# Kernel tuning notes

Measured on AMD Instinct MI355X. Metric: run time of the kernel, lower is better.

## Reference

```python
import jax, jax.numpy as jnp
import numpy as np

N, F, A = 50000, 128, 128

def setup_inputs() -> dict:
    key = jax.random.key(0)
    ks = jax.random.split(key, 20)
    r = lambda i, shape: jax.random.normal(ks[i], shape, dtype=jnp.float32)
    w = lambda i, shape: jax.random.normal(ks[i], shape, dtype=jnp.float32) * 0.05
    return {
        "feat": r(0, (N, F)),
        "mu": r(1, (N, F, 3)),
        "T0": r(2, (N,)),
        "T1": r(3, (N, 3)),
        "T2": r(4, (N, 3, 3)),
        "T3": r(5, (N, 3, 3, 3)),
        # denseq: Dense(F,F,swish) -> Dense(F,F). Weights stored [in,out].
        "Wq1": w(6, (F, F)), "bq1": jnp.zeros((F,), jnp.float32),
        "Wq2": w(7, (F, F)), "bq2": jnp.zeros((F,), jnp.float32),
        "WT1": w(8, (F, F)),  # dense_T1, no bias
        "WT2": w(9, (F, F)),  # dense_T2, no bias
        "WT3": w(10, (F, F)), # dense_T3, no bias
        # dense_s: Dense(F,F,swish) -> Dense(F,A)
        "Ws1": w(11, (F, F)), "bs1": jnp.zeros((F,), jnp.float32),
        "Ws2": w(12, (F, A)), "bs2": jnp.zeros((A,), jnp.float32),
        "Wv": w(13, (F, A)),  # dense_v, no bias
    }

def reference(feat, mu, T0, T1, T2, T3,
              Wq1, bq1, Wq2, bq2, WT1, WT2, WT3,
              Ws1, bs1, Ws2, bs2, Wv):
    silu = jax.nn.silu  # swish
    # M0 = denseq(feat): [N, F]
    M0 = silu(feat @ Wq1 + bq1) @ Wq2 + bq2
    # M1/M2/M3: linear over feature dim of mu [N, F, 3]
    M1 = jnp.einsum('nfc,fg->ngc', mu, WT1)
    M2 = jnp.einsum('nfc,fg->ngc', mu, WT2)
    M3 = jnp.einsum('nfc,fg->ngc', mu, WT3)
    # scalar channel
    ms = jnp.sum(M1 * T1[:, None, :], axis=-1) + T0[:, None] * M0          # T1, T0 terms
    ms = ms + jnp.einsum('nfi,nfj,nij->nf', M2, M2, T2)                    # quadrupole . T2
    ms = ms + jnp.einsum('nfi,nfj,nfk,nijk->nf', M3, M3, M3, T3)           # octupole . T3
    # vector channel [N, F, 3]
    mv = T1[:, None, :] * M0[..., None]
    mv = mv + jnp.einsum('nij,nfj->nfi', T2, M1)
    mv = mv + jnp.einsum('nijk,nfj,nfk->nfi', T3, M2, M2)
    # output projections
    mv_out = jnp.einsum('nfc,fa->nac', mv, Wv)                             # [N, A, 3]
    ms_out = silu(ms @ Ws1 + bs1) @ Ws2 + bs2                              # [N, A]
    return ms_out, mv_out
```

## Files before the change

kernel.cpp:

```cpp
#include <hip/hip_runtime.h>
#include <cstdint>

#define N_NODES 50000
#define TILE 32
#define NBLK ((N_NODES + TILE - 1) / TILE)

typedef __bf16 bf16x8 __attribute__((ext_vector_type(8)));
typedef unsigned short ushort8_t __attribute__((ext_vector_type(8)));
typedef float f32x4 __attribute__((ext_vector_type(4)));

__device__ __forceinline__ unsigned short f2bf(float x) {
  union { float f; uint32_t u; } v; v.f = x;
  uint32_t r = v.u + 0x7FFFu + ((v.u >> 16) & 1u);
  return (unsigned short)(r >> 16);
}

__device__ __forceinline__ float fast_silu(float x) {
  return x / (1.0f + __expf(-x));
}

__global__ __launch_bounds__(256) void prep_weights(
    const float* __restrict__ Wq1, const float* __restrict__ Wq2,
    const float* __restrict__ WT1, const float* __restrict__ WT2,
    const float* __restrict__ WT3, const float* __restrict__ Ws1,
    const float* __restrict__ Ws2, const float* __restrict__ Wv,
    unsigned short* __restrict__ ws) {
  int tid = blockIdx.x * 256 + threadIdx.x;
  int w = tid >> 11;
  int rest = tid & 2047;
  int c = rest >> 8;
  int kt = (rest >> 6) & 3;
  int lane = rest & 63;
  int g = (lane & 15) + 16 * c;
  int k0 = kt * 32 + (lane >> 4) * 8;
  const float* srcs[8] = {Wq1, Wq2, WT1, WT2, WT3, Ws1, Ws2, Wv};
  const float* src = srcs[w];
  union { unsigned short u[8]; uint4 v; } o;
#pragma unroll
  for (int j = 0; j < 8; ++j) o.u[j] = f2bf(src[(k0 + j) * 128 + g]);
  *(uint4*)(ws + (size_t)w * 16384 + (size_t)rest * 8) = o.v;
}

__device__ __forceinline__ void gemm16(const unsigned short* sA,
                                       const unsigned short* sWp,
                                       int lane, int cb, f32x4 acc[2][2]) {
  const int m = lane & 15, q = lane >> 4;
  const f32x4 vzero = {0.f, 0.f, 0.f, 0.f};
#pragma unroll
  for (int rt = 0; rt < 2; ++rt)
#pragma unroll
    for (int cc = 0; cc < 2; ++cc) acc[rt][cc] = vzero;
#pragma unroll
  for (int kt = 0; kt < 4; ++kt) {
    const int k0 = q * 8 + kt * 32;
    bf16x8 a0 = __builtin_bit_cast(bf16x8, *(const ushort8_t*)(sA + m * 136 + k0));
    bf16x8 a1 = __builtin_bit_cast(bf16x8, *(const ushort8_t*)(sA + (m + 16) * 136 + k0));
#pragma unroll
    for (int cc = 0; cc < 2; ++cc) {
      bf16x8 b = __builtin_bit_cast(
          bf16x8, *(const ushort8_t*)(sWp + (((cb + cc) * 4 + kt) * 64 + lane) * 8));
      acc[0][cc] = __builtin_amdgcn_mfma_f32_16x16x32_bf16(a0, b, acc[0][cc], 0, 0, 0);
      acc[1][cc] = __builtin_amdgcn_mfma_f32_16x16x32_bf16(a1, b, acc[1][cc], 0, 0, 0);
    }
  }
}

__global__ __launch_bounds__(256, 2) void multipole_main(
    const float* __restrict__ feat, const float* __restrict__ mu,
    const float* __restrict__ T0g, const float* __restrict__ T1g,
    const float* __restrict__ T2g, const float* __restrict__ T3g,
    const float* __restrict__ bq1, const float* __restrict__ bq2,
    const float* __restrict__ bs1, const float* __restrict__ bs2,
    const unsigned short* __restrict__ ws, float* __restrict__ out) {
  __shared__ unsigned short sW[16384];
  __shared__ unsigned short sXmain[TILE * 136];
  __shared__ unsigned short sXmu[3][TILE * 136];
  __shared__ float sT[TILE][49];

  const int t = threadIdx.x;
  const int lane = t & 63, wv = t >> 6;
  const int m = lane & 15, q = lane >> 4;
  const int cb = wv * 2;
  const int nodeBase = blockIdx.x * TILE;

  auto stage_w = [&](int slot) {
    const uint4* src = (const uint4*)(ws + (size_t)slot * 16384);
    uint4* dst = (uint4*)sW;
#pragma unroll
    for (int i = 0; i < 8; ++i) dst[t + i * 256] = src[t + i * 256];
  };

  if (t < TILE) {
    int n = nodeBase + t;
    bool val = n < N_NODES;
    float t0 = val ? T0g[n] : 0.f;
    float t1[3], t2[9], t3[27];
#pragma unroll
    for (int i = 0; i < 3; ++i) t1[i] = val ? T1g[n * 3 + i] : 0.f;
#pragma unroll
    for (int i = 0; i < 9; ++i) t2[i] = val ? T2g[n * 9 + i] : 0.f;
#pragma unroll
    for (int i = 0; i < 27; ++i) t3[i] = val ? T3g[n * 27 + i] : 0.f;
    float* Tr = sT[t];
    Tr[0] = t0;
    Tr[1] = t1[0]; Tr[2] = t1[1]; Tr[3] = t1[2];
#pragma unroll
    for (int i = 0; i < 9; ++i) Tr[4 + i] = t2[i];
    Tr[13] = t2[0]; Tr[14] = t2[1] + t2[3]; Tr[15] = t2[2] + t2[6];
    Tr[16] = t2[4]; Tr[17] = t2[5] + t2[7]; Tr[18] = t2[8];
    Tr[19] = t3[0];
    Tr[20] = t3[1] + t3[3] + t3[9];
    Tr[21] = t3[2] + t3[6] + t3[18];
    Tr[22] = t3[4] + t3[10] + t3[12];
    Tr[23] = t3[5] + t3[7] + t3[11] + t3[15] + t3[19] + t3[21];
    Tr[24] = t3[8] + t3[20] + t3[24];
    Tr[25] = t3[13];
    Tr[26] = t3[14] + t3[16] + t3[22];
    Tr[27] = t3[17] + t3[23] + t3[25];
    Tr[28] = t3[26];
#pragma unroll
    for (int i = 0; i < 3; ++i) {
      const float* b = t3 + 9 * i;
      float* d = Tr + 29 + 6 * i;
      d[0] = b[0]; d[1] = b[1] + b[3]; d[2] = b[2] + b[6];
      d[3] = b[4]; d[4] = b[5] + b[7]; d[5] = b[8];
    }
  }

  {
    int node = t >> 3, f0 = (t & 7) * 16;
    int gn = nodeBase + node;
    union { unsigned short u[16]; uint4 v[2]; } buf;
    if (gn < N_NODES) {
      const float* p = feat + (size_t)gn * 128 + f0;
#pragma unroll
      for (int i = 0; i < 16; ++i) buf.u[i] = f2bf(p[i]);
    } else {
#pragma unroll
      for (int i = 0; i < 16; ++i) buf.u[i] = 0;
    }
    uint4* dst = (uint4*)&sXmain[node * 136 + f0];
    dst[0] = buf.v[0]; dst[1] = buf.v[1];
  }
  stage_w(0);
  __syncthreads();

  f32x4 A1[2][2], A2[2][2], A3[2][2];
  float msv[2][2][4];
  float mvv[3][2][2][4];

  gemm16(sXmain, sW, lane, cb, A1);
  float b0 = bq1[cb * 16 + m], b1 = bq1[cb * 16 + 16 + m];
  __syncthreads();
#pragma unroll
  for (int rt = 0; rt < 2; ++rt)
#pragma unroll
    for (int ri = 0; ri < 4; ++ri) {
      int lrow = rt * 16 + q * 4 + ri;
#pragma unroll
      for (int cc = 0; cc < 2; ++cc) {
        float h = fast_silu(A1[rt][cc][ri] + (cc ? b1 : b0));
        sXmain[lrow * 136 + (cb + cc) * 16 + m] = f2bf(h);
      }
    }
  stage_w(1);
  __syncthreads();

  gemm16(sXmain, sW, lane, cb, A1);
  {
    float bb0 = bq2[cb * 16 + m], bb1 = bq2[cb * 16 + 16 + m];
#pragma unroll
    for (int rt = 0; rt < 2; ++rt)
#pragma unroll
      for (int ri = 0; ri < 4; ++ri) {
        const float* Tr = sT[rt * 16 + q * 4 + ri];
        float t0 = Tr[0], ta = Tr[1], tb = Tr[2], tc = Tr[3];
#pragma unroll
        for (int cc = 0; cc < 2; ++cc) {
          float m0 = A1[rt][cc][ri] + (cc ? bb1 : bb0);
          msv[rt][cc][ri] = t0 * m0;
          mvv[0][rt][cc][ri] = ta * m0;
          mvv[1][rt][cc][ri] = tb * m0;
          mvv[2][rt][cc][ri] = tc * m0;
        }
      }
  }
  __syncthreads();

  {
    int node = t >> 3, f0 = (t & 7) * 16;
    int gn = nodeBase + node;
    union { unsigned short u[16]; uint4 v[2]; } b3[3];
    if (gn < N_NODES) {
      const float* p = mu + ((size_t)gn * 128 + f0) * 3;
#pragma unroll
      for (int i = 0; i < 16; ++i) {
        b3[0].u[i] = f2bf(p[i * 3 + 0]);
        b3[1].u[i] = f2bf(p[i * 3 + 1]);
        b3[2].u[i] = f2bf(p[i * 3 + 2]);
      }
    } else {
#pragma unroll
      for (int ch = 0; ch < 3; ++ch)
#pragma unroll
        for (int i = 0; i < 16; ++i) b3[ch].u[i] = 0;
    }
#pragma unroll
    for (int ch = 0; ch < 3; ++ch) {
      uint4* dst = (uint4*)&sXmu[ch][node * 136 + f0];
      dst[0] = b3[ch].v[0]; dst[1] = b3[ch].v[1];
    }
  }
  stage_w(2);
  __syncthreads();

#pragma unroll
  for (int ch = 0; ch < 3; ++ch) {
    gemm16(sXmu[ch], sW, lane, cb, A1);
#pragma unroll
    for (int rt = 0; rt < 2; ++rt)
#pragma unroll
      for (int ri = 0; ri < 4; ++ri) {
        const float* Tr = sT[rt * 16 + q * 4 + ri];
        float t1c = Tr[1 + ch];
        float u0 = Tr[4 + 0 + ch], u1 = Tr[4 + 3 + ch], u2 = Tr[4 + 6 + ch];
#pragma unroll
        for (int cc = 0; cc < 2; ++cc) {
          float v = A1[rt][cc][ri];
          msv[rt][cc][ri] += t1c * v;
          mvv[0][rt][cc][ri] += u0 * v;
          mvv[1][rt][cc][ri] += u1 * v;
          mvv[2][rt][cc][ri] += u2 * v;
        }
      }
  }
  __syncthreads();
  stage_w(4);
  __syncthreads();

  gemm16(sXmu[0], sW, lane, cb, A1);
  gemm16(sXmu[1], sW, lane, cb, A2);
  gemm16(sXmu[2], sW, lane, cb, A3);
#pragma unroll
  for (int rt = 0; rt < 2; ++rt)
#pragma unroll
    for (int ri = 0; ri < 4; ++ri) {
      const float* Cp = sT[rt * 16 + q * 4 + ri] + 19;
      float c0 = Cp[0], c1 = Cp[1], c2 = Cp[2], c3 = Cp[3], c4 = Cp[4];
      float c5 = Cp[5], c6 = Cp[6], c7 = Cp[7], c8 = Cp[8], c9 = Cp[9];
#pragma unroll
      for (int cc = 0; cc < 2; ++cc) {
        float u0 = A1[rt][cc][ri], u1 = A2[rt][cc][ri], u2 = A3[rt][cc][ri];
        float Q0 = u0 * u0, Q1 = u0 * u1, Q2 = u0 * u2;
        float Q3 = u1 * u1, Q4 = u1 * u2, Q5 = u2 * u2;
        msv[rt][cc][ri] += c0 * (Q0 * u0) + c1 * (Q0 * u1) + c2 * (Q0 * u2) +
                           c3 * (Q1 * u1) + c4 * (Q1 * u2) + c5 * (Q2 * u2) +
                           c6 * (Q3 * u1) + c7 * (Q3 * u2) + c8 * (Q4 * u2) +
                           c9 * (Q5 * u2);
      }
    }
  __syncthreads();
  stage_w(3);
  __syncthreads();

  gemm16(sXmu[0], sW, lane, cb, A1);
  gemm16(sXmu[1], sW, lane, cb, A2);
  gemm16(sXmu[2], sW, lane, cb, A3);
#pragma unroll
  for (int rt = 0; rt < 2; ++rt)
#pragma unroll
    for (int ri = 0; ri < 4; ++ri) {
      const float* Tr = sT[rt * 16 + q * 4 + ri];
      const float* q2 = Tr + 13;
      const float* d3 = Tr + 29;
      float q20 = q2[0], q21 = q2[1], q22 = q2[2], q23 = q2[3], q24 = q2[4], q25 = q2[5];
#pragma unroll
      for (int cc = 0; cc < 2; ++cc) {
        float v0 = A1[rt][cc][ri], v1 = A2[rt][cc][ri], v2 = A3[rt][cc][ri];
        float P0 = v0 * v0, P1 = v0 * v1, P2 = v0 * v2;
        float P3 = v1 * v1, P4 = v1 * v2, P5 = v2 * v2;
        msv[rt][cc][ri] += q20 * P0 + q21 * P1 + q22 * P2 + q23 * P3 + q24 * P4 + q25 * P5;
        mvv[0][rt][cc][ri] += d3[0] * P0 + d3[1] * P1 + d3[2] * P2 + d3[3] * P3 + d3[4] * P4 + d3[5] * P5;
        mvv[1][rt][cc][ri] += d3[6] * P0 + d3[7] * P1 + d3[8] * P2 + d3[9] * P3 + d3[10] * P4 + d3[11] * P5;
        mvv[2][rt][cc][ri] += d3[12] * P0 + d3[13] * P1 + d3[14] * P2 + d3[15] * P3 + d3[16] * P4 + d3[17] * P5;
      }
    }
  __syncthreads();

#pragma unroll
  for (int rt = 0; rt < 2; ++rt)
#pragma unroll
    for (int ri = 0; ri < 4; ++ri) {
      int lrow = rt * 16 + q * 4 + ri;
#pragma unroll
      for (int cc = 0; cc < 2; ++cc) {
        int col = (cb + cc) * 16 + m;
        sXmain[lrow * 136 + col] = f2bf(msv[rt][cc][ri]);
        sXmu[0][lrow * 136 + col] = f2bf(mvv[0][rt][cc][ri]);
        sXmu[1][lrow * 136 + col] = f2bf(mvv[1][rt][cc][ri]);
        sXmu[2][lrow * 136 + col] = f2bf(mvv[2][rt][cc][ri]);
      }
    }
  stage_w(5);
  __syncthreads();

  gemm16(sXmain, sW, lane, cb, A1);
  {
    float s0 = bs1[cb * 16 + m], s1 = bs1[cb * 16 + 16 + m];
    __syncthreads();
#pragma unroll
    for (int rt = 0; rt < 2; ++rt)
#pragma unroll
      for (int ri = 0; ri < 4; ++ri) {
        int lrow = rt * 16 + q * 4 + ri;
#pragma unroll
        for (int cc = 0; cc < 2; ++cc) {
          float g = fast_silu(A1[rt][cc][ri] + (cc ? s1 : s0));
          sXmain[lrow * 136 + (cb + cc) * 16 + m] = f2bf(g);
        }
      }
  }
  stage_w(6);
  __syncthreads();

  gemm16(sXmain, sW, lane, cb, A1);
  {
    float s0 = bs2[cb * 16 + m], s1 = bs2[cb * 16 + 16 + m];
#pragma unroll
    for (int rt = 0; rt < 2; ++rt)
#pragma unroll
      for (int ri = 0; ri < 4; ++ri) {
        int grow = nodeBase + rt * 16 + q * 4 + ri;
        if (grow < N_NODES) {
#pragma unroll
          for (int cc = 0; cc < 2; ++cc) {
            int col = (cb + cc) * 16 + m;
            out[(size_t)grow * 128 + col] = A1[rt][cc][ri] + (cc ? s1 : s0);
          }
        }
      }
  }
  __syncthreads();
  stage_w(7);
  __syncthreads();

  float* out2 = out + (size_t)N_NODES * 128;
#pragma unroll
  for (int ch = 0; ch < 3; ++ch) {
    gemm16(sXmu[ch], sW, lane, cb, A1);
#pragma unroll
    for (int rt = 0; rt < 2; ++rt)
#pragma unroll
      for (int ri = 0; ri < 4; ++ri) {
        int grow = nodeBase + rt * 16 + q * 4 + ri;
        if (grow < N_NODES) {
#pragma unroll
          for (int cc = 0; cc < 2; ++cc) {
            int col = (cb + cc) * 16 + m;
            out2[((size_t)grow * 128 + col) * 3 + ch] = A1[rt][cc][ri];
          }
        }
      }
  }
}

extern "C" void kernel_launch(void* const* d_in, const int* in_sizes, int n_in,
                              void* d_out, int out_size, void* d_ws, size_t ws_size,
                              hipStream_t stream) {
  const float* feat = (const float*)d_in[0];
  const float* mu   = (const float*)d_in[1];
  const float* T0   = (const float*)d_in[2];
  const float* T1   = (const float*)d_in[3];
  const float* T2   = (const float*)d_in[4];
  const float* T3   = (const float*)d_in[5];
  const float* Wq1  = (const float*)d_in[6];
  const float* bq1  = (const float*)d_in[7];
  const float* Wq2  = (const float*)d_in[8];
  const float* bq2  = (const float*)d_in[9];
  const float* WT1  = (const float*)d_in[10];
  const float* WT2  = (const float*)d_in[11];
  const float* WT3  = (const float*)d_in[12];
  const float* Ws1  = (const float*)d_in[13];
  const float* bs1  = (const float*)d_in[14];
  const float* Ws2  = (const float*)d_in[15];
  const float* bs2  = (const float*)d_in[16];
  const float* Wv   = (const float*)d_in[17];
  unsigned short* ws = (unsigned short*)d_ws;
  float* out = (float*)d_out;

  prep_weights<<<64, 256, 0, stream>>>(Wq1, Wq2, WT1, WT2, WT3, Ws1, Ws2, Wv, ws);
  multipole_main<<<NBLK, 256, 0, stream>>>(feat, mu, T0, T1, T2, T3,
                                           bq1, bq2, bs1, bs2, ws, out);
}
```

Measured before the change: 275.8 us.

## Read MFMA weight fragments from global memory instead of staging through LDS

Removes the 32KB shared weight buffer and its per-stage copies and barriers. MFMA B fragments now load directly from the prepacked global workspace, where they should hit L2 or cache. This frees LDS and raises the occupancy target to 4 blocks per CU. Input loads for feat and mu are vectorized as float4 and hoisted to the kernel start, and the final Wv projection is fused across the three channels so all three components of each output are written together. The risk is extra global/L2 traffic and load latency on every GEMM.

```diff
diff --git a/kernel.cpp b/kernel.cpp
--- a/kernel.cpp
+++ b/kernel.cpp
@@ -41,9 +41,15 @@
   *(uint4*)(ws + (size_t)w * 16384 + (size_t)rest * 8) = o.v;
 }
 
-__device__ __forceinline__ void gemm16(const unsigned short* sA,
-                                       const unsigned short* sWp,
-                                       int lane, int cb, f32x4 acc[2][2]) {
+__device__ __forceinline__ bf16x8 ldB(const unsigned short* __restrict__ wg,
+                                      int c, int kt, int lane) {
+  return __builtin_bit_cast(
+      bf16x8, *(const ushort8_t*)(wg + (((c * 4 + kt) * 64 + lane)) * 8));
+}
+
+__device__ __forceinline__ void gemm16g(const unsigned short* __restrict__ sA,
+                                        const unsigned short* __restrict__ wg,
+                                        int lane, int cb, f32x4 acc[2][2]) {
   const int m = lane & 15, q = lane >> 4;
   const f32x4 vzero = {0.f, 0.f, 0.f, 0.f};
 #pragma unroll
@@ -57,25 +63,60 @@
     bf16x8 a1 = __builtin_bit_cast(bf16x8, *(const ushort8_t*)(sA + (m + 16) * 136 + k0));
 #pragma unroll
     for (int cc = 0; cc < 2; ++cc) {
-      bf16x8 b = __builtin_bit_cast(
-          bf16x8, *(const ushort8_t*)(sWp + (((cb + cc) * 4 + kt) * 64 + lane) * 8));
+      bf16x8 b = ldB(wg, cb + cc, kt, lane);
       acc[0][cc] = __builtin_amdgcn_mfma_f32_16x16x32_bf16(a0, b, acc[0][cc], 0, 0, 0);
       acc[1][cc] = __builtin_amdgcn_mfma_f32_16x16x32_bf16(a1, b, acc[1][cc], 0, 0, 0);
     }
   }
 }
 
-__global__ __launch_bounds__(256, 2) void multipole_main(
+__device__ __forceinline__ void gemm3g(const unsigned short* __restrict__ s0,
+                                       const unsigned short* __restrict__ s1,
+                                       const unsigned short* __restrict__ s2,
+                                       const unsigned short* __restrict__ wg,
+                                       int lane, int cb,
+                                       f32x4 A1[2][2], f32x4 A2[2][2],
+                                       f32x4 A3[2][2]) {
+  const int m = lane & 15, q = lane >> 4;
+  const f32x4 vzero = {0.f, 0.f, 0.f, 0.f};
+#pragma unroll
+  for (int rt = 0; rt < 2; ++rt)
+#pragma unroll
+    for (int cc = 0; cc < 2; ++cc) {
+      A1[rt][cc] = vzero; A2[rt][cc] = vzero; A3[rt][cc] = vzero;
+    }
+#pragma unroll
+  for (int kt = 0; kt < 4; ++kt) {
+    const int k0 = q * 8 + kt * 32;
+    bf16x8 a00 = __builtin_bit_cast(bf16x8, *(const ushort8_t*)(s0 + m * 136 + k0));
+    bf16x8 a01 = __builtin_bit_cast(bf16x8, *(const ushort8_t*)(s0 + (m + 16) * 136 + k0));
+    bf16x8 a10 = __builtin_bit_cast(bf16x8, *(const ushort8_t*)(s1 + m * 136 + k0));
+    bf16x8 a11 = __builtin_bit_cast(bf16x8, *(const ushort8_t*)(s1 + (m + 16) * 136 + k0));
+    bf16x8 a20 = __builtin_bit_cast(bf16x8, *(const ushort8_t*)(s2 + m * 136 + k0));
+    bf16x8 a21 = __builtin_bit_cast(bf16x8, *(const ushort8_t*)(s2 + (m + 16) * 136 + k0));
+#pragma unroll
+    for (int cc = 0; cc < 2; ++cc) {
+      bf16x8 b = ldB(wg, cb + cc, kt, lane);
+      A1[0][cc] = __builtin_amdgcn_mfma_f32_16x16x32_bf16(a00, b, A1[0][cc], 0, 0, 0);
+      A1[1][cc] = __builtin_amdgcn_mfma_f32_16x16x32_bf16(a01, b, A1[1][cc], 0, 0, 0);
+      A2[0][cc] = __builtin_amdgcn_mfma_f32_16x16x32_bf16(a10, b, A2[0][cc], 0, 0, 0);
+      A2[1][cc] = __builtin_amdgcn_mfma_f32_16x16x32_bf16(a11, b, A2[1][cc], 0, 0, 0);
+      A3[0][cc] = __builtin_amdgcn_mfma_f32_16x16x32_bf16(a20, b, A3[0][cc], 0, 0, 0);
+      A3[1][cc] = __builtin_amdgcn_mfma_f32_16x16x32_bf16(a21, b, A3[1][cc], 0, 0, 0);
+    }
+  }
+}
+
+__global__ __launch_bounds__(256, 4) void multipole_main(
     const float* __restrict__ feat, const float* __restrict__ mu,
     const float* __restrict__ T0g, const float* __restrict__ T1g,
     const float* __restrict__ T2g, const float* __restrict__ T3g,
     const float* __restrict__ bq1, const float* __restrict__ bq2,
     const float* __restrict__ bs1, const float* __restrict__ bs2,
     const unsigned short* __restrict__ ws, float* __restrict__ out) {
-  __shared__ unsigned short sW[16384];
   __shared__ unsigned short sXmain[TILE * 136];
   __shared__ unsigned short sXmu[3][TILE * 136];
-  __shared__ float sT[TILE][49];
+  __shared__ float sT[TILE][47];
 
   const int t = threadIdx.x;
   const int lane = t & 63, wv = t >> 6;
@@ -83,12 +124,52 @@
   const int cb = wv * 2;
   const int nodeBase = blockIdx.x * TILE;
 
-  auto stage_w = [&](int slot) {
-    const uint4* src = (const uint4*)(ws + (size_t)slot * 16384);
-    uint4* dst = (uint4*)sW;
-#pragma unroll
-    for (int i = 0; i < 8; ++i) dst[t + i * 256] = src[t + i * 256];
-  };
+  {
+    int node = t >> 3, f0 = (t & 7) * 16;
+    int gn = nodeBase + node;
+    union { unsigned short u[16]; uint4 v[2]; } buf;
+    if (gn < N_NODES) {
+      const float4* p = (const float4*)(feat + (size_t)gn * 128 + f0);
+      float xs[16];
+#pragma unroll
+      for (int i = 0; i < 4; ++i) *(float4*)(xs + 4 * i) = p[i];
+#pragma unroll
+      for (int i = 0; i < 16; ++i) buf.u[i] = f2bf(xs[i]);
+    } else {
+#pragma unroll
+      for (int i = 0; i < 16; ++i) buf.u[i] = 0;
+    }
+    uint4* dst = (uint4*)&sXmain[node * 136 + f0];
+    dst[0] = buf.v[0]; dst[1] = buf.v[1];
+  }
+
+  {
+    int node = t >> 3, f0 = (t & 7) * 16;
+    int gn = nodeBase + node;
+    union { unsigned short u[16]; uint4 v[2]; } b3[3];
+    if (gn < N_NODES) {
+      const float4* p = (const float4*)(mu + ((size_t)gn * 128 + f0) * 3);
+      float xs[48];
+#pragma unroll
+      for (int i = 0; i < 12; ++i) *(float4*)(xs + 4 * i) = p[i];
+#pragma unroll
+      for (int i = 0; i < 16; ++i) {
+        b3[0].u[i] = f2bf(xs[i * 3 + 0]);
+        b3[1].u[i] = f2bf(xs[i * 3 + 1]);
+        b3[2].u[i] = f2bf(xs[i * 3 + 2]);
+      }
+    } else {
+#pragma unroll
+      for (int ch = 0; ch < 3; ++ch)
+#pragma unroll
+        for (int i = 0; i < 16; ++i) b3[ch].u[i] = 0;
+    }
+#pragma unroll
+    for (int ch = 0; ch < 3; ++ch) {
+      uint4* dst = (uint4*)&sXmu[ch][node * 136 + f0];
+      dst[0] = b3[ch].v[0]; dst[1] = b3[ch].v[1];
+    }
+  }
 
   if (t < TILE) {
     int n = nodeBase + t;
@@ -126,30 +207,13 @@
       d[3] = b[4]; d[4] = b[5] + b[7]; d[5] = b[8];
     }
   }
-
-  {
-    int node = t >> 3, f0 = (t & 7) * 16;
-    int gn = nodeBase + node;
-    union { unsigned short u[16]; uint4 v[2]; } buf;
-    if (gn < N_NODES) {
-      const float* p = feat + (size_t)gn * 128 + f0;
-#pragma unroll
-      for (int i = 0; i < 16; ++i) buf.u[i] = f2bf(p[i]);
-    } else {
-#pragma unroll
-      for (int i = 0; i < 16; ++i) buf.u[i] = 0;
-    }
-    uint4* dst = (uint4*)&sXmain[node * 136 + f0];
-    dst[0] = buf.v[0]; dst[1] = buf.v[1];
-  }
-  stage_w(0);
   __syncthreads();
 
   f32x4 A1[2][2], A2[2][2], A3[2][2];
   float msv[2][2][4];
   float mvv[3][2][2][4];
 
-  gemm16(sXmain, sW, lane, cb, A1);
+  gemm16g(sXmain, ws, lane, cb, A1);
   float b0 = bq1[cb * 16 + m], b1 = bq1[cb * 16 + 16 + m];
   __syncthreads();
 #pragma unroll
@@ -163,10 +227,9 @@
         sXmain[lrow * 136 + (cb + cc) * 16 + m] = f2bf(h);
       }
     }
-  stage_w(1);
-  __syncthreads();
-
-  gemm16(sXmain, sW, lane, cb, A1);
+  __syncthreads();
+
+  gemm16g(sXmain, ws + 1 * 16384, lane, cb, A1);
   {
     float bb0 = bq2[cb * 16 + m], bb1 = bq2[cb * 16 + 16 + m];
 #pragma unroll
@@ -185,38 +248,10 @@
         }
       }
   }
-  __syncthreads();
-
-  {
-    int node = t >> 3, f0 = (t & 7) * 16;
-    int gn = nodeBase + node;
-    union { unsigned short u[16]; uint4 v[2]; } b3[3];
-    if (gn < N_NODES) {
-      const float* p = mu + ((size_t)gn * 128 + f0) * 3;
-#pragma unroll
-      for (int i = 0; i < 16; ++i) {
-        b3[0].u[i] = f2bf(p[i * 3 + 0]);
-        b3[1].u[i] = f2bf(p[i * 3 + 1]);
-        b3[2].u[i] = f2bf(p[i * 3 + 2]);
-      }
-    } else {
-#pragma unroll
-      for (int ch = 0; ch < 3; ++ch)
-#pragma unroll
-        for (int i = 0; i < 16; ++i) b3[ch].u[i] = 0;
-    }
-#pragma unroll
-    for (int ch = 0; ch < 3; ++ch) {
-      uint4* dst = (uint4*)&sXmu[ch][node * 136 + f0];
-      dst[0] = b3[ch].v[0]; dst[1] = b3[ch].v[1];
-    }
-  }
-  stage_w(2);
-  __syncthreads();
 
 #pragma unroll
   for (int ch = 0; ch < 3; ++ch) {
-    gemm16(sXmu[ch], sW, lane, cb, A1);
+    gemm16g(sXmu[ch], ws + 2 * 16384, lane, cb, A1);
 #pragma unroll
     for (int rt = 0; rt < 2; ++rt)
 #pragma unroll
@@ -234,13 +269,10 @@
         }
       }
   }
-  __syncthreads();
-  stage_w(4);
-  __syncthreads();
-
-  gemm16(sXmu[0], sW, lane, cb, A1);
-  gemm16(sXmu[1], sW, lane, cb, A2);
-  gemm16(sXmu[2], sW, lane, cb, A3);
+
+  gemm16g(sXmu[0], ws + 4 * 16384, lane, cb, A1);
+  gemm16g(sXmu[1], ws + 4 * 16384, lane, cb, A2);
+  gemm16g(sXmu[2], ws + 4 * 16384, lane, cb, A3);
 #pragma unroll
   for (int rt = 0; rt < 2; ++rt)
 #pragma unroll
@@ -259,13 +291,10 @@
                            c9 * (Q5 * u2);
       }
     }
-  __syncthreads();
-  stage_w(3);
-  __syncthreads();
-
-  gemm16(sXmu[0], sW, lane, cb, A1);
-  gemm16(sXmu[1], sW, lane, cb, A2);
-  gemm16(sXmu[2], sW, lane, cb, A3);
+
+  gemm16g(sXmu[0], ws + 3 * 16384, lane, cb, A1);
+  gemm16g(sXmu[1], ws + 3 * 16384, lane, cb, A2);
+  gemm16g(sXmu[2], ws + 3 * 16384, lane, cb, A3);
 #pragma unroll
   for (int rt = 0; rt < 2; ++rt)
 #pragma unroll
@@ -301,10 +330,9 @@
         sXmu[2][lrow * 136 + col] = f2bf(mvv[2][rt][cc][ri]);
       }
     }
-  stage_w(5);
-  __syncthreads();
-
-  gemm16(sXmain, sW, lane, cb, A1);
+  __syncthreads();
+
+  gemm16g(sXmain, ws + 5 * 16384, lane, cb, A1);
   {
     float s0 = bs1[cb * 16 + m], s1 = bs1[cb * 16 + 16 + m];
     __syncthreads();
@@ -320,10 +348,9 @@
         }
       }
   }
-  stage_w(6);
-  __syncthreads();
-
-  gemm16(sXmain, sW, lane, cb, A1);
+  __syncthreads();
+
+  gemm16g(sXmain, ws + 6 * 16384, lane, cb, A1);
   {
     float s0 = bs2[cb * 16 + m], s1 = bs2[cb * 16 + 16 + m];
 #pragma unroll
@@ -340,28 +367,25 @@
         }
       }
   }
-  __syncthreads();
-  stage_w(7);
-  __syncthreads();
 
   float* out2 = out + (size_t)N_NODES * 128;
-#pragma unroll
-  for (int ch = 0; ch < 3; ++ch) {
-    gemm16(sXmu[ch], sW, lane, cb, A1);
-#pragma unroll
-    for (int rt = 0; rt < 2; ++rt)
-#pragma unroll
-      for (int ri = 0; ri < 4; ++ri) {
-        int grow = nodeBase + rt * 16 + q * 4 + ri;
-        if (grow < N_NODES) {
-#pragma unroll
-          for (int cc = 0; cc < 2; ++cc) {
-            int col = (cb + cc) * 16 + m;
-            out2[((size_t)grow * 128 + col) * 3 + ch] = A1[rt][cc][ri];
-          }
+  gemm3g(sXmu[0], sXmu[1], sXmu[2], ws + 7 * 16384, lane, cb, A1, A2, A3);
+#pragma unroll
+  for (int rt = 0; rt < 2; ++rt)
+#pragma unroll
+    for (int ri = 0; ri < 4; ++ri) {
+      int grow = nodeBase + rt * 16 + q * 4 + ri;
+      if (grow < N_NODES) {
+#pragma unroll
+        for (int cc = 0; cc < 2; ++cc) {
+          int col = (cb + cc) * 16 + m;
+          float* p = out2 + ((size_t)grow * 128 + col) * 3;
+          p[0] = A1[rt][cc][ri];
+          p[1] = A2[rt][cc][ri];
+          p[2] = A3[rt][cc][ri];
         }
       }
-  }
+    }
 }
 
 extern "C" void kernel_launch(void* const* d_in, const int* in_sizes, int n_in,
```

Result: slower. 501.1 us (+81.7%).
